# Kernel tuning notes

Hardware: AMD Instinct MI355X
Metric: run time of the kernel (lower is better)

## Reference

```python
import jax, jax.numpy as jnp
import numpy as np

N = 100000       # nodes
E = 1600000      # edges (avg degree 16)
D_IN = 6         # in_node_dim
HID = 128        # hidden_dim (heads=1)
OUT = 2          # output_dim
NEG_SLOPE = 0.2  # PyG GATConv leaky_relu slope


def setup_inputs() -> dict:
    key = jax.random.key(0)
    ks = jax.random.split(key, 16)
    inp = {
        "x": jax.random.normal(ks[0], (N, D_IN), dtype=jnp.float32),
        "edge_index": jax.random.randint(ks[1], (2, E), 0, N, dtype=jnp.int64),
        "edge_weight": jax.random.uniform(ks[2], (E, 1), dtype=jnp.float32),
        # GATConv params (heads=1, out=HID)
        "w_gat": jax.random.normal(ks[3], (D_IN, HID), dtype=jnp.float32) * 0.1,
        "att_src": jax.random.normal(ks[4], (HID,), dtype=jnp.float32) * 0.1,
        "att_dst": jax.random.normal(ks[5], (HID,), dtype=jnp.float32) * 0.1,
        "w_edge": jax.random.normal(ks[6], (1, HID), dtype=jnp.float32) * 0.1,
        "att_edge": jax.random.normal(ks[7], (HID,), dtype=jnp.float32) * 0.1,
        "b_gat": jax.random.normal(ks[8], (HID,), dtype=jnp.float32) * 0.01,
        # GCNConv params
        "w_gcn": jax.random.normal(ks[9], (HID, HID), dtype=jnp.float32) * 0.05,
        "b_gcn": jax.random.normal(ks[10], (HID,), dtype=jnp.float32) * 0.01,
        # output Linear
        "w_out": jax.random.normal(ks[11], (HID, OUT), dtype=jnp.float32) * 0.05,
        "b_out": jax.random.normal(ks[12], (OUT,), dtype=jnp.float32) * 0.01,
    }
    return inp


def _segment_softmax(logits, seg, num_segments):
    # numerically stable softmax over edges grouped by destination node
    m = jax.ops.segment_max(logits, seg, num_segments=num_segments)
    m = jnp.where(jnp.isfinite(m), m, 0.0)  # empty segments
    e = jnp.exp(logits - m[seg])
    denom = jax.ops.segment_sum(e, seg, num_segments=num_segments)
    return e / jnp.clip(denom, 1e-16)[seg]


def reference(x, edge_weight, w_gat, att_src, att_dst, w_edge, att_edge,
              b_gat, w_gcn, b_gcn, w_out, b_out, edge_index):
    x = x.astype(jnp.float32)
    edge_weight = edge_weight.astype(jnp.float32)
    src, dst = edge_index[0], edge_index[1]

    # ---- GATConv (heads=1, edge_dim=1, no self loops) ----
    h = x @ w_gat                              # [N, HID]
    a_src = h @ att_src                        # [N]
    a_dst = h @ att_dst                        # [N]
    e_feat = edge_weight @ w_edge              # [E, HID]
    a_edge = e_feat @ att_edge                 # [E]
    logits = jax.nn.leaky_relu(a_src[src] + a_dst[dst] + a_edge, NEG_SLOPE)
    alpha = _segment_softmax(logits, dst, N)   # [E], attention weights
    h_gat = jax.ops.segment_sum(alpha[:, None] * h[src], dst, num_segments=N)
    h_gat = h_gat + b_gat                      # [N, HID]
    h1 = jax.nn.relu(h_gat)

    # ---- GCNConv with edge_weight = alpha (no self loops, symmetric norm) ----
    deg = jax.ops.segment_sum(alpha, dst, num_segments=N)  # [N]
    dinv = jnp.where(deg > 0, deg ** -0.5, 0.0)
    norm = dinv[src] * alpha * dinv[dst]       # [E]
    hx = h1 @ w_gcn                            # [N, HID]
    h2 = jax.ops.segment_sum(norm[:, None] * hx[src], dst, num_segments=N)
    h2 = jax.nn.relu(h2 + b_gcn)

    # ---- output head ----
    out = h2 @ w_out + b_out                   # [N, OUT]
    return out, edge_index, alpha
```

## Files before the change

### kernel.cpp

```cpp
#include <hip/hip_runtime.h>
#include <hip/hip_bf16.h>
#include <math.h>

#define N_NODES 100000
#define N_EDGES 1600000
#define HID 128
#define D_IN 6
#define NEG_SLOPE 0.2f

#define NB_BKT 128
#define NBKT 782
#define NBLK_P 200
#define EPB ((N_EDGES + NBLK_P - 1) / NBLK_P)
#define NHIST (NBKT * NBLK_P)
#define S2_CAP 3072

__global__ __launch_bounds__(128) void k_prep(
    const float* __restrict__ w_gat, const float* __restrict__ att_src,
    const float* __restrict__ att_dst, const float* __restrict__ w_edge,
    const float* __restrict__ att_edge, float* __restrict__ w_as,
    float* __restrict__ w_ad, float* __restrict__ dotwe)
{
    int tid = threadIdx.x;
    __shared__ float red[4];
    float as = att_src[tid], ad = att_dst[tid];

    float v = w_edge[tid] * att_edge[tid];
    for (int o = 32; o; o >>= 1) v += __shfl_down(v, o);
    if ((tid & 63) == 0) red[tid >> 6] = v;
    __syncthreads();
    if (tid == 0) dotwe[0] = red[0] + red[1];

#pragma unroll
    for (int i = 0; i < D_IN; ++i) {
        float wv = w_gat[i * HID + tid];
        float v1 = wv * as, v2 = wv * ad;
        for (int o = 32; o; o >>= 1) {
            v1 += __shfl_down(v1, o);
            v2 += __shfl_down(v2, o);
        }
        __syncthreads();
        if ((tid & 63) == 0) { red[(tid >> 6) * 2] = v1; red[(tid >> 6) * 2 + 1] = v2; }
        __syncthreads();
        if (tid == 0) { w_as[i] = red[0] + red[2]; w_ad[i] = red[1] + red[3]; }
    }
}

__global__ __launch_bounds__(256) void k_asrc(
    const float* __restrict__ x, const float* __restrict__ w_as,
    const float* __restrict__ w_ad, float* __restrict__ a_src,
    float* __restrict__ a_dst)
{
    int n = blockIdx.x * 256 + threadIdx.x;
    if (n >= N_NODES) return;
    float s0 = 0.f, s1 = 0.f;
#pragma unroll
    for (int i = 0; i < D_IN; ++i) {
        float xv = x[n * D_IN + i];
        s0 += xv * w_as[i];
        s1 += xv * w_ad[i];
    }
    a_src[n] = s0;
    a_dst[n] = s1;
}

__global__ __launch_bounds__(256) void k_hist(
    const int* __restrict__ dst, int* __restrict__ histG)
{
    __shared__ int h[NBKT];
    for (int b = threadIdx.x; b < NBKT; b += 256) h[b] = 0;
    __syncthreads();
    int e0 = blockIdx.x * EPB, e1 = min(e0 + EPB, N_EDGES);
    for (int e = e0 + threadIdx.x; e < e1; e += 256)
        atomicAdd(&h[dst[e] >> 7], 1);
    __syncthreads();
    for (int b = threadIdx.x; b < NBKT; b += 256)
        histG[b * NBLK_P + blockIdx.x] = h[b];
}

__global__ __launch_bounds__(512) void k_scan1(
    const int* __restrict__ in, int* __restrict__ incl, int* __restrict__ bsums,
    int n)
{
    __shared__ int s[512];
    int tid = threadIdx.x;
    int i = blockIdx.x * 512 + tid;
    int v = (i < n) ? in[i] : 0;
    s[tid] = v;
    __syncthreads();
    for (int o = 1; o < 512; o <<= 1) {
        int t = (tid >= o) ? s[tid - o] : 0;
        __syncthreads();
        s[tid] += t;
        __syncthreads();
    }
    if (i < n) incl[i] = s[tid];
    if (tid == 511) bsums[blockIdx.x] = s[511];
}

__global__ __launch_bounds__(512) void k_scan2(
    const int* __restrict__ bsums, int* __restrict__ boffs, int nb)
{
    __shared__ int s[512];
    int tid = threadIdx.x;
    int v = (tid < nb) ? bsums[tid] : 0;
    s[tid] = v;
    __syncthreads();
    for (int o = 1; o < 512; o <<= 1) {
        int t = (tid >= o) ? s[tid - o] : 0;
        __syncthreads();
        s[tid] += t;
        __syncthreads();
    }
    if (tid < nb) boffs[tid] = s[tid] - v;
}

__global__ __launch_bounds__(512) void k_scan3(
    const int* __restrict__ in, const int* __restrict__ incl,
    const int* __restrict__ boffs, int* __restrict__ off, int n)
{
    int i = blockIdx.x * 512 + threadIdx.x;
    if (i < n) {
        int b = boffs[blockIdx.x];
        off[i] = b + incl[i] - in[i];
        if (i == n - 1) off[n] = b + incl[i];
    }
}

__global__ __launch_bounds__(256) void k_part(
    const int* __restrict__ src, const int* __restrict__ dst,
    const float* __restrict__ ew, const float* __restrict__ a_src,
    const float* __restrict__ a_dst, const float* __restrict__ dotwe,
    const int* __restrict__ offP, float* __restrict__ p_arr,
    uint2* __restrict__ rec)
{
    __shared__ int curs[NBKT];
    for (int b = threadIdx.x; b < NBKT; b += 256)
        curs[b] = offP[b * NBLK_P + blockIdx.x];
    __syncthreads();
    float dw = dotwe[0];
    int e0 = blockIdx.x * EPB, e1 = min(e0 + EPB, N_EDGES);
    for (int e = e0 + threadIdx.x; e < e1; e += 256) {
        int d = dst[e], s = src[e];
        float lg = a_src[s] + a_dst[d] + dw * ew[e];
        lg = (lg >= 0.f) ? lg : NEG_SLOPE * lg;
        float p = __expf(lg);
        p_arr[e] = p;
        int pos = atomicAdd(&curs[d >> 7], 1);
        rec[pos] = make_uint2(((unsigned)(d & 127) << 17) | (unsigned)s,
                              __float_as_uint(p));
    }
}

__global__ __launch_bounds__(256) void k_s2(
    const int* __restrict__ offP, const uint2* __restrict__ rec,
    const float* __restrict__ x, uint2* __restrict__ sa_srt,
    float* __restrict__ xagg8, float* __restrict__ denomG,
    int* __restrict__ off)
{
    __shared__ uint2 srt[S2_CAP];
    __shared__ int cntL[NB_BKT], fillL[NB_BKT], baseL[NB_BKT + 1];
    __shared__ int sc[NB_BKT];
    __shared__ float rden[NB_BKT];
    int b = blockIdx.x, tid = threadIdx.x;
    int g0 = offP[b * NBLK_P];
    int g1 = offP[(b + 1) * NBLK_P];
    int len = min(g1 - g0, S2_CAP);

    if (tid < NB_BKT) { cntL[tid] = 0; fillL[tid] = 0; }
    __syncthreads();

    for (int i = tid; i < len; i += 256)
        atomicAdd(&cntL[rec[g0 + i].x >> 17], 1);
    __syncthreads();

    {
        int v = (tid < NB_BKT) ? cntL[tid] : 0;
        if (tid < NB_BKT) sc[tid] = v;
        __syncthreads();
        for (int o = 1; o < NB_BKT; o <<= 1) {
            int t = (tid >= o && tid < NB_BKT) ? sc[tid - o] : 0;
            __syncthreads();
            if (tid < NB_BKT) sc[tid] += t;
            __syncthreads();
        }
        if (tid < NB_BKT) baseL[tid + 1] = sc[tid];
        if (tid == 0) baseL[0] = 0;
    }
    __syncthreads();

    for (int i = tid; i < len; i += 256) {
        uint2 r = rec[g0 + i];
        int dl = r.x >> 17;
        int p = baseL[dl] + atomicAdd(&fillL[dl], 1);
        if (p < S2_CAP) srt[p] = r;
    }
    __syncthreads();

    if (tid < NB_BKT) {
        int s0 = baseL[tid], s1 = baseL[tid + 1];
        float dsum = 0.f;
        for (int j = s0; j < s1; ++j) dsum += __uint_as_float(srt[j].y);
        int n = b * NB_BKT + tid;
        if (n < N_NODES) denomG[n] = dsum;
        rden[tid] = 1.0f / fmaxf(dsum, 1e-16f);
    }
    __syncthreads();

    for (int i = tid; i < len; i += 256) {
        uint2 r = srt[i];
        int dl = r.x >> 17;
        float a = __uint_as_float(r.y) * rden[dl];
        srt[i].y = __float_as_uint(a);
        sa_srt[g0 + i] = make_uint2(r.x & 0x1FFFFu, __float_as_uint(a));
    }
    __syncthreads();

    if (tid < NB_BKT) {
        int n = b * NB_BKT + tid;
        if (n < N_NODES) {
            int s0 = baseL[tid], s1 = baseL[tid + 1];
            float ax0 = 0, ax1 = 0, ax2 = 0, ax3 = 0, ax4 = 0, ax5 = 0;
            for (int j = s0; j < s1; ++j) {
                uint2 r = srt[j];
                float a = __uint_as_float(r.y);
                const float2* xp = (const float2*)(x + (size_t)(r.x & 0x1FFFFu) * D_IN);
                float2 q0 = xp[0], q1 = xp[1], q2 = xp[2];
                ax0 += a * q0.x; ax1 += a * q0.y; ax2 += a * q1.x;
                ax3 += a * q1.y; ax4 += a * q2.x; ax5 += a * q2.y;
            }
            float dv = (s1 > s0) ? 1.0f : 0.0f;
            float* xo = xagg8 + (size_t)n * 8;
            float4 lo = {dv, ax0, ax1, ax2};
            float4 hi = {ax3, ax4, ax5, 0.f};
            *(float4*)xo = lo;
            *(float4*)(xo + 4) = hi;
            off[n] = g0 + s0;
        }
    }
    if (b == NBKT - 1 && tid == 0) off[N_NODES] = g1;
}

__global__ __launch_bounds__(256) void k_alpha(
    const float* __restrict__ p_arr, const int* __restrict__ dst,
    const float* __restrict__ denomG, float* __restrict__ alpha_out)
{
    int e = blockIdx.x * 256 + threadIdx.x;
    if (e >= N_EDGES) return;
    alpha_out[e] = p_arr[e] / fmaxf(denomG[dst[e]], 1e-16f);
}

#define GCAP 128
__global__ __launch_bounds__(256) void k_gcn_gather(
    const uint2* __restrict__ sa_srt, const int* __restrict__ off,
    const float* __restrict__ xagg8, const float* __restrict__ w_gat,
    const float* __restrict__ b_gat, float* __restrict__ agg)
{
    __shared__ float lds[GCAP * 12];
    int tid = threadIdx.x;
    int n0 = blockIdx.x * 4;
    int wid = tid >> 6, l = tid & 63;
    int n = n0 + wid;
    int beg0 = off[n0];
    int total = off[n0 + 4] - beg0;
    int nb = off[n] - beg0, ne = off[n + 1] - beg0;

    int kA = l, kB = l + 64;
    float wA0 = w_gat[0 * HID + kA], wA1 = w_gat[1 * HID + kA], wA2 = w_gat[2 * HID + kA];
    float wA3 = w_gat[3 * HID + kA], wA4 = w_gat[4 * HID + kA], wA5 = w_gat[5 * HID + kA];
    float wB0 = w_gat[0 * HID + kB], wB1 = w_gat[1 * HID + kB], wB2 = w_gat[2 * HID + kB];
    float wB3 = w_gat[3 * HID + kB], wB4 = w_gat[4 * HID + kB], wB5 = w_gat[5 * HID + kB];
    float bA = b_gat[kA], bB = b_gat[kB];
    float accA = 0.f, accB = 0.f;

    for (int base = 0; base < total; base += GCAP) {
        int cnt = min(GCAP, total - base);
        __syncthreads();
        if (tid < cnt) {
            int j = beg0 + base + tid;
            uint2 sa = sa_srt[j];
            float a = __uint_as_float(sa.y);
            const float4* xp = (const float4*)(xagg8 + (size_t)sa.x * 8);
            float4 lo = xp[0], hi = xp[1];
            float4 w0 = {lo.x * a, lo.y, lo.z, lo.w};
            float4 w1 = {hi.x, hi.y, hi.z, 0.f};
            *(float4*)(lds + tid * 12) = w0;
            *(float4*)(lds + tid * 12 + 4) = w1;
        }
        __syncthreads();
        int lo_t = nb - base; if (lo_t < 0) lo_t = 0;
        int hi_t = ne - base; if (hi_t > cnt) hi_t = cnt;
        for (int t = lo_t; t < hi_t; ++t) {
            float4 e0 = *(const float4*)(lds + t * 12);
            float4 e1 = *(const float4*)(lds + t * 12 + 4);
            float hA = bA, hB = bB;
            hA = fmaf(e0.y, wA0, hA); hB = fmaf(e0.y, wB0, hB);
            hA = fmaf(e0.z, wA1, hA); hB = fmaf(e0.z, wB1, hB);
            hA = fmaf(e0.w, wA2, hA); hB = fmaf(e0.w, wB2, hB);
            hA = fmaf(e1.x, wA3, hA); hB = fmaf(e1.x, wB3, hB);
            hA = fmaf(e1.y, wA4, hA); hB = fmaf(e1.y, wB4, hB);
            hA = fmaf(e1.z, wA5, hA); hB = fmaf(e1.z, wB5, hB);
            hA = fmaxf(hA, 0.f); hB = fmaxf(hB, 0.f);
            accA = fmaf(e0.x, hA, accA); accB = fmaf(e0.x, hB, accB);
        }
    }
    float dn = xagg8[(size_t)n * 8];
    agg[(size_t)n * HID + kA] = dn * accA;
    agg[(size_t)n * HID + kB] = dn * accB;
}

#define NPB 32
#define HSTR (NPB + 4)
__global__ __launch_bounds__(128) void k_dense2(
    const float* __restrict__ agg, const float* __restrict__ w_gcn,
    const float* __restrict__ b_gcn, const float* __restrict__ w_out,
    const float* __restrict__ b_out, float* __restrict__ out)
{
    __shared__ float hT[HID][HSTR];
    int tid = threadIdx.x;
    int n0 = blockIdx.x * NPB;

#pragma unroll
    for (int r = 0; r < NPB; ++r)
        hT[tid][r] = agg[(size_t)(n0 + r) * HID + tid];
    __syncthreads();

    int c0 = tid & 15;
    int r0 = (tid >> 4) * 4;

    float acc[4][8];
#pragma unroll
    for (int r = 0; r < 4; ++r)
#pragma unroll
        for (int j = 0; j < 8; ++j) acc[r][j] = 0.f;

    const float* wp = w_gcn + c0;
#pragma unroll 2
    for (int i = 0; i < HID; ++i) {
        float4 hv = *(const float4*)&hT[i][r0];
        float w[8];
#pragma unroll
        for (int j = 0; j < 8; ++j) w[j] = wp[i * HID + 16 * j];
#pragma unroll
        for (int j = 0; j < 8; ++j) {
            acc[0][j] = fmaf(hv.x, w[j], acc[0][j]);
            acc[1][j] = fmaf(hv.y, w[j], acc[1][j]);
            acc[2][j] = fmaf(hv.z, w[j], acc[2][j]);
            acc[3][j] = fmaf(hv.w, w[j], acc[3][j]);
        }
    }

    float po[4][2];
#pragma unroll
    for (int r = 0; r < 4; ++r) { po[r][0] = 0.f; po[r][1] = 0.f; }
#pragma unroll
    for (int j = 0; j < 8; ++j) {
        int c = c0 + 16 * j;
        float b = b_gcn[c];
        float w0 = w_out[c * 2 + 0], w1 = w_out[c * 2 + 1];
#pragma unroll
        for (int r = 0; r < 4; ++r) {
            float h2 = fmaxf(acc[r][j] + b, 0.f);
            po[r][0] = fmaf(h2, w0, po[r][0]);
            po[r][1] = fmaf(h2, w1, po[r][1]);
        }
    }

#pragma unroll
    for (int r = 0; r < 4; ++r)
#pragma unroll
        for (int o = 0; o < 2; ++o) {
            float v = po[r][o];
            v += __shfl_xor(v, 1);
            v += __shfl_xor(v, 2);
            v += __shfl_xor(v, 4);
            v += __shfl_xor(v, 8);
            po[r][o] = v;
        }
    if ((tid & 15) == 0) {
        float b0 = b_out[0], b1 = b_out[1];
#pragma unroll
        for (int r = 0; r < 4; ++r) {
            out[(size_t)(n0 + r0 + r) * 2 + 0] = po[r][0] + b0;
            out[(size_t)(n0 + r0 + r) * 2 + 1] = po[r][1] + b1;
        }
    }
}

__global__ __launch_bounds__(256) void k_copy_ei(
    const int* __restrict__ ei, float* __restrict__ out_ei)
{
    int i = blockIdx.x * 256 + threadIdx.x;
    if (i < (2 * N_EDGES) / 4) {
        int4 v = ((const int4*)ei)[i];
        float4 f = {(float)v.x, (float)v.y, (float)v.z, (float)v.w};
        ((float4*)out_ei)[i] = f;
    }
}

extern "C" void kernel_launch(void* const* d_in, const int* in_sizes, int n_in,
                              void* d_out, int out_size, void* d_ws, size_t ws_size,
                              hipStream_t stream)
{
    const float* x        = (const float*)d_in[0];
    const int*   ei       = (const int*)d_in[1];
    const float* ew       = (const float*)d_in[2];
    const float* w_gat    = (const float*)d_in[3];
    const float* att_src  = (const float*)d_in[4];
    const float* att_dst  = (const float*)d_in[5];
    const float* w_edge   = (const float*)d_in[6];
    const float* att_edge = (const float*)d_in[7];
    const float* b_gat    = (const float*)d_in[8];
    const float* w_gcn    = (const float*)d_in[9];
    const float* b_gcn    = (const float*)d_in[10];
    const float* w_out    = (const float*)d_in[11];
    const float* b_out    = (const float*)d_in[12];

    const int* src = ei;
    const int* dst = ei + N_EDGES;

    float* out_head  = (float*)d_out;
    float* out_ei    = out_head + 2 * N_NODES;
    float* out_alpha = out_ei + 2 * N_EDGES;

    char* ws = (char*)d_ws;
    size_t o = 0;
    auto alloc = [&](size_t bytes) -> char* {
        char* p = ws + o;
        o = (o + bytes + 255) & ~(size_t)255;
        return p;
    };
    float* agg    = (float*)alloc((size_t)N_NODES * HID * 4);
    uint2* rec    = (uint2*)alloc((size_t)N_EDGES * 8);
    uint2* sa_srt = (uint2*)alloc((size_t)N_EDGES * 8);
    float* p_arr  = (float*)alloc((size_t)N_EDGES * 4);
    float* xagg8  = (float*)alloc((size_t)N_NODES * 8 * 4);
    int*   histG  = (int*)alloc((size_t)NHIST * 4);
    int*   incl   = (int*)alloc((size_t)NHIST * 4);
    int*   offP   = (int*)alloc((size_t)(NHIST + 1) * 4);
    float* a_src  = (float*)alloc(N_NODES * 4);
    float* a_dst  = (float*)alloc(N_NODES * 4);
    float* denomG = (float*)alloc(N_NODES * 4);
    int*   off    = (int*)alloc((N_NODES + 1) * 4);
    int*   bsums  = (int*)alloc(512 * 4);
    int*   boffs  = (int*)alloc(512 * 4);
    float* w_as   = (float*)alloc(D_IN * 4);
    float* w_ad   = (float*)alloc(D_IN * 4);
    float* dotwe  = (float*)alloc(4);
    (void)ws_size; (void)out_size; (void)n_in; (void)in_sizes;

    const int NB_NODE = (N_NODES + 255) / 256;
    const int NB_EDGE = (N_EDGES + 255) / 256;
    const int NB_SCANP = (NHIST + 511) / 512;

    k_prep<<<1, 128, 0, stream>>>(w_gat, att_src, att_dst, w_edge, att_edge,
                                  w_as, w_ad, dotwe);
    k_asrc<<<NB_NODE, 256, 0, stream>>>(x, w_as, w_ad, a_src, a_dst);
    k_hist<<<NBLK_P, 256, 0, stream>>>(dst, histG);
    k_scan1<<<NB_SCANP, 512, 0, stream>>>(histG, incl, bsums, NHIST);
    k_scan2<<<1, 512, 0, stream>>>(bsums, boffs, NB_SCANP);
    k_scan3<<<NB_SCANP, 512, 0, stream>>>(histG, incl, boffs, offP, NHIST);
    k_part<<<NBLK_P, 256, 0, stream>>>(src, dst, ew, a_src, a_dst, dotwe,
                                       offP, p_arr, rec);
    k_s2<<<NBKT, 256, 0, stream>>>(offP, rec, x, sa_srt, xagg8, denomG, off);
    k_alpha<<<NB_EDGE, 256, 0, stream>>>(p_arr, dst, denomG, out_alpha);
    k_gcn_gather<<<N_NODES / 4, 256, 0, stream>>>(
        sa_srt, off, xagg8, w_gat, b_gat, agg);
    k_dense2<<<N_NODES / NPB, 128, 0, stream>>>(
        agg, w_gcn, b_gcn, w_out, b_out, out_head);
    k_copy_ei<<<(2 * N_EDGES) / 4 / 256 + 1, 256, 0, stream>>>(ei, out_ei);
}
```

Before: 294.7 us.

## Retile dense GCN matmul into 128x128 blocked GEMM with LDS-staged weights

```diff
diff --git a/kernel.cpp b/kernel.cpp
--- a/kernel.cpp
+++ b/kernel.cpp
@@ -250,7 +250,7 @@
     alpha_out[e] = p_arr[e] / fmaxf(denomG[dst[e]], 1e-16f);
 }
 
-#define GCAP 128
+#define GCAP 256
 __global__ __launch_bounds__(256) void k_gcn_gather(
     const uint2* __restrict__ sa_srt, const int* __restrict__ off,
     const float* __restrict__ xagg8, const float* __restrict__ w_gat,
@@ -309,80 +309,93 @@
     agg[(size_t)n * HID + kB] = dn * accB;
 }
 
-#define NPB 32
-#define HSTR (NPB + 4)
-__global__ __launch_bounds__(128) void k_dense2(
+#define DM 128
+#define DK 32
+__global__ __launch_bounds__(256, 4) void k_dense2(
     const float* __restrict__ agg, const float* __restrict__ w_gcn,
     const float* __restrict__ b_gcn, const float* __restrict__ w_out,
     const float* __restrict__ b_out, float* __restrict__ out)
 {
-    __shared__ float hT[HID][HSTR];
+    __shared__ float As[DK][DM + 4];
+    __shared__ float Bs[DK][HID];
     int tid = threadIdx.x;
-    int n0 = blockIdx.x * NPB;
-
-#pragma unroll
-    for (int r = 0; r < NPB; ++r)
-        hT[tid][r] = agg[(size_t)(n0 + r) * HID + tid];
-    __syncthreads();
-
-    int c0 = tid & 15;
-    int r0 = (tid >> 4) * 4;
-
-    float acc[4][8];
-#pragma unroll
-    for (int r = 0; r < 4; ++r)
+    int m0 = blockIdx.x * DM;
+    int tx = tid & 15;
+    int ty = tid >> 4;
+
+    float acc[8][8];
+#pragma unroll
+    for (int r = 0; r < 8; ++r)
 #pragma unroll
         for (int j = 0; j < 8; ++j) acc[r][j] = 0.f;
 
-    const float* wp = w_gcn + c0;
-#pragma unroll 2
-    for (int i = 0; i < HID; ++i) {
-        float4 hv = *(const float4*)&hT[i][r0];
-        float w[8];
-#pragma unroll
-        for (int j = 0; j < 8; ++j) w[j] = wp[i * HID + 16 * j];
+    for (int k0 = 0; k0 < HID; k0 += DK) {
+#pragma unroll
+        for (int q = 0; q < 4; ++q) {
+            int idx4 = tid + q * 256;
+            int m = idx4 >> 3;
+            int k4 = (idx4 & 7) * 4;
+            int gm = m0 + m;
+            float4 v = (gm < N_NODES)
+                ? *(const float4*)(agg + (size_t)gm * HID + k0 + k4)
+                : make_float4(0.f, 0.f, 0.f, 0.f);
+            As[k4 + 0][m] = v.x;
+            As[k4 + 1][m] = v.y;
+            As[k4 + 2][m] = v.z;
+            As[k4 + 3][m] = v.w;
+        }
+#pragma unroll
+        for (int q = 0; q < 4; ++q) {
+            int idx4 = tid + q * 256;
+            int k = idx4 >> 5;
+            int n4 = (idx4 & 31) * 4;
+            *(float4*)&Bs[k][n4] = *(const float4*)(w_gcn + (size_t)(k0 + k) * HID + n4);
+        }
+        __syncthreads();
+#pragma unroll 4
+        for (int k = 0; k < DK; ++k) {
+            float4 w0 = *(const float4*)&Bs[k][tx * 8];
+            float4 w1 = *(const float4*)&Bs[k][tx * 8 + 4];
+            float4 h0 = *(const float4*)&As[k][ty * 8];
+            float4 h1 = *(const float4*)&As[k][ty * 8 + 4];
+            float hv[8] = {h0.x, h0.y, h0.z, h0.w, h1.x, h1.y, h1.z, h1.w};
+            float wv[8] = {w0.x, w0.y, w0.z, w0.w, w1.x, w1.y, w1.z, w1.w};
+#pragma unroll
+            for (int r = 0; r < 8; ++r)
+#pragma unroll
+                for (int j = 0; j < 8; ++j)
+                    acc[r][j] = fmaf(hv[r], wv[j], acc[r][j]);
+        }
+        __syncthreads();
+    }
+
+    float bb[8], wo0[8], wo1[8];
+#pragma unroll
+    for (int j = 0; j < 8; ++j) {
+        int c = tx * 8 + j;
+        bb[j] = b_gcn[c];
+        wo0[j] = w_out[c * 2 + 0];
+        wo1[j] = w_out[c * 2 + 1];
+    }
+#pragma unroll
+    for (int r = 0; r < 8; ++r) {
+        float p0 = 0.f, p1 = 0.f;
 #pragma unroll
         for (int j = 0; j < 8; ++j) {
-            acc[0][j] = fmaf(hv.x, w[j], acc[0][j]);
-            acc[1][j] = fmaf(hv.y, w[j], acc[1][j]);
-            acc[2][j] = fmaf(hv.z, w[j], acc[2][j]);
-            acc[3][j] = fmaf(hv.w, w[j], acc[3][j]);
-        }
-    }
-
-    float po[4][2];
-#pragma unroll
-    for (int r = 0; r < 4; ++r) { po[r][0] = 0.f; po[r][1] = 0.f; }
-#pragma unroll
-    for (int j = 0; j < 8; ++j) {
-        int c = c0 + 16 * j;
-        float b = b_gcn[c];
-        float w0 = w_out[c * 2 + 0], w1 = w_out[c * 2 + 1];
-#pragma unroll
-        for (int r = 0; r < 4; ++r) {
-            float h2 = fmaxf(acc[r][j] + b, 0.f);
-            po[r][0] = fmaf(h2, w0, po[r][0]);
-            po[r][1] = fmaf(h2, w1, po[r][1]);
-        }
-    }
-
-#pragma unroll
-    for (int r = 0; r < 4; ++r)
-#pragma unroll
-        for (int o = 0; o < 2; ++o) {
-            float v = po[r][o];
-            v += __shfl_xor(v, 1);
-            v += __shfl_xor(v, 2);
-            v += __shfl_xor(v, 4);
-            v += __shfl_xor(v, 8);
-            po[r][o] = v;
-        }
-    if ((tid & 15) == 0) {
-        float b0 = b_out[0], b1 = b_out[1];
-#pragma unroll
-        for (int r = 0; r < 4; ++r) {
-            out[(size_t)(n0 + r0 + r) * 2 + 0] = po[r][0] + b0;
-            out[(size_t)(n0 + r0 + r) * 2 + 1] = po[r][1] + b1;
+            float h2 = fmaxf(acc[r][j] + bb[j], 0.f);
+            p0 = fmaf(h2, wo0[j], p0);
+            p1 = fmaf(h2, wo1[j], p1);
+        }
+        p0 += __shfl_xor(p0, 1);  p1 += __shfl_xor(p1, 1);
+        p0 += __shfl_xor(p0, 2);  p1 += __shfl_xor(p1, 2);
+        p0 += __shfl_xor(p0, 4);  p1 += __shfl_xor(p1, 4);
+        p0 += __shfl_xor(p0, 8);  p1 += __shfl_xor(p1, 8);
+        if (tx == 0) {
+            int gm = m0 + ty * 8 + r;
+            if (gm < N_NODES) {
+                out[(size_t)gm * 2 + 0] = p0 + b_out[0];
+                out[(size_t)gm * 2 + 1] = p1 + b_out[1];
+            }
         }
     }
 }
@@ -466,7 +479,7 @@
     k_alpha<<<NB_EDGE, 256, 0, stream>>>(p_arr, dst, denomG, out_alpha);
     k_gcn_gather<<<N_NODES / 4, 256, 0, stream>>>(
         sa_srt, off, xagg8, w_gat, b_gat, agg);
-    k_dense2<<<N_NODES / NPB, 128, 0, stream>>>(
+    k_dense2<<<(N_NODES + DM - 1) / DM, 256, 0, stream>>>(
         agg, w_gcn, b_gcn, w_out, b_out, out_head);
     k_copy_ei<<<(2 * N_EDGES) / 4 / 256 + 1, 256, 0, stream>>>(ei, out_ei);
 }
```

Measured after the change: 303.7 us. 1.03x slower.
